# Kernel optimization log

Measured on AMD Instinct MI355X. Metric: run time of the kernel, lower is better.

Reference implementation:

```python
import jax, jax.numpy as jnp
import numpy as np

B, T, C = 2, 2048, 2048
H, D = 16, 128


def _rope(x, cos, sin):
    # x: [B,H,T,D], cos/sin: [T,D//2]
    half = x.shape[-1] // 2
    x1, x2 = x[..., :half], x[..., half:]
    c = cos[None, None, :, :]
    s = sin[None, None, :, :]
    return jnp.concatenate([x1 * c - x2 * s, x1 * s + x2 * c], axis=-1)


def setup_inputs() -> dict:
    key = jax.random.key(0)
    k1, k2, k3, k4, k5 = jax.random.split(key, 5)
    x = jax.random.normal(k1, (B, T, C), dtype=jnp.float32)
    cos = jax.random.uniform(k2, (T, D // 2), dtype=jnp.float32)
    sin = jax.random.uniform(k3, (T, D // 2), dtype=jnp.float32)
    scale = 1.0 / np.sqrt(C)
    W_qkv = jax.random.normal(k4, (C, 3 * C), dtype=jnp.float32) * scale
    W_proj = jax.random.normal(k5, (C, C), dtype=jnp.float32) * scale
    return {"x": x, "cos": cos, "sin": sin, "W_qkv": W_qkv, "W_proj": W_proj}


def reference(x, cos, sin, W_qkv, W_proj):
    Bx, Tx, Cx = x.shape
    qkv = x @ W_qkv  # [B,T,3C]
    q, k, v = jnp.split(qkv, 3, axis=-1)
    # [B,T,C] -> [B,H,T,D]
    q = q.reshape(Bx, Tx, H, D).transpose(0, 2, 1, 3)
    k = k.reshape(Bx, Tx, H, D).transpose(0, 2, 1, 3)
    v = v.reshape(Bx, Tx, H, D).transpose(0, 2, 1, 3)
    q = _rope(q, cos, sin)
    k = _rope(k, cos, sin)
    # causal SDPA
    scores = jnp.einsum("bhqd,bhkd->bhqk", q, k) / jnp.sqrt(jnp.float32(D))
    causal = jnp.tril(jnp.ones((Tx, Tx), dtype=bool))
    scores = jnp.where(causal[None, None], scores, jnp.finfo(scores.dtype).min)
    attn = jax.nn.softmax(scores, axis=-1)
    out = jnp.einsum("bhqk,bhkd->bhqd", attn, v)
    out = out.transpose(0, 2, 1, 3).reshape(Bx, Tx, Cx)
    return out @ W_proj
```

## Files before the change

### kernel.cpp

```cpp
#include <hip/hip_runtime.h>
#include <stdint.h>

#define B_  2
#define T_  2048
#define C_  2048
#define H_  16
#define D_  128
#define BH_ 32
#define M_  4096

typedef __attribute__((ext_vector_type(8))) __bf16  bf16x8;
typedef __attribute__((ext_vector_type(4))) float   floatx4;
typedef __attribute__((ext_vector_type(4))) ushort  ushortx4;

__device__ __forceinline__ ushort f2bf(float f) {
    union { float f; uint32_t u; } v; v.f = f;
    return (ushort)((v.u + 0x7fffu + ((v.u >> 16) & 1u)) >> 16);
}

__device__ __forceinline__ floatx4 mfma_bf16(bf16x8 a, bf16x8 b, floatx4 c) {
    return __builtin_amdgcn_mfma_f32_16x16x32_bf16(a, b, c, 0, 0, 0);
}

__device__ __forceinline__ void async16(const ushort* g, ushort* l) {
    __builtin_amdgcn_global_load_lds(
        (const __attribute__((address_space(1))) uint32_t*)g,
        (__attribute__((address_space(3))) uint32_t*)l, 16, 0, 0);
}

__global__ __launch_bounds__(256) void transpose_w(
    const float* __restrict__ W, ushort* __restrict__ Wt, int Kdim, int Ndim)
{
    __shared__ float tile[32][33];
    const int n0 = blockIdx.x * 32, k0 = blockIdx.y * 32;
    const int tx = threadIdx.x, ty = threadIdx.y;
    #pragma unroll
    for (int j = 0; j < 4; j++)
        tile[ty + j*8][tx] = W[(size_t)(k0 + ty + j*8) * Ndim + n0 + tx];
    __syncthreads();
    #pragma unroll
    for (int j = 0; j < 4; j++)
        Wt[(size_t)(n0 + ty + j*8) * Kdim + k0 + tx] = f2bf(tile[tx][ty + j*8]);
}

#define BM 128
#define BN 128
#define BK 32
#define LDK 40

__global__ __launch_bounds__(256) void gemm_af32_btbf16(
    const float* __restrict__ A, const ushort* __restrict__ Bt,
    float* __restrict__ Co, int Ndim, int Kdim)
{
    __shared__ __align__(16) ushort As[BM * LDK];
    __shared__ __align__(16) ushort Bs[BN * LDK];
    const int tid  = threadIdx.x;
    const int lane = tid & 63;
    const int w    = tid >> 6;
    const int wm   = (w >> 1) * 64;
    const int wn   = (w & 1) * 64;
    const int lr   = lane & 15;
    const int quad = lane >> 4;

    const float*  Ablk = A  + (size_t)(blockIdx.y * BM) * Kdim;
    const ushort* Bblk = Bt + (size_t)(blockIdx.x * BN) * Kdim;

    floatx4 acc[4][4];
    #pragma unroll
    for (int i = 0; i < 4; i++)
        #pragma unroll
        for (int j = 0; j < 4; j++)
            acc[i][j] = (floatx4){0.f, 0.f, 0.f, 0.f};

    for (int k0 = 0; k0 < Kdim; k0 += BK) {
        #pragma unroll
        for (int i = 0; i < 4; i++) {
            int idx = tid + i * 256;
            int row = idx >> 3;
            int c4  = (idx & 7) * 4;
            const float4 a = *(const float4*)(Ablk + (size_t)row * Kdim + k0 + c4);
            ushortx4 p = { f2bf(a.x), f2bf(a.y), f2bf(a.z), f2bf(a.w) };
            *(ushortx4*)(&As[row * LDK + c4]) = p;
        }
        #pragma unroll
        for (int i = 0; i < 2; i++) {
            int idx = tid + i * 256;
            int row = idx >> 2;
            int c8  = (idx & 3) * 8;
            bf16x8 bv = *(const bf16x8*)(Bblk + (size_t)row * Kdim + k0 + c8);
            *(bf16x8*)(&Bs[row * LDK + c8]) = bv;
        }
        __syncthreads();

        bf16x8 af[4], bfr[4];
        #pragma unroll
        for (int mi = 0; mi < 4; mi++)
            af[mi] = *(const bf16x8*)(&As[(wm + mi*16 + lr) * LDK + quad * 8]);
        #pragma unroll
        for (int ni = 0; ni < 4; ni++)
            bfr[ni] = *(const bf16x8*)(&Bs[(wn + ni*16 + lr) * LDK + quad * 8]);
        #pragma unroll
        for (int mi = 0; mi < 4; mi++)
            #pragma unroll
            for (int ni = 0; ni < 4; ni++)
                acc[mi][ni] = mfma_bf16(af[mi], bfr[ni], acc[mi][ni]);
        __syncthreads();
    }

    const size_t row0 = (size_t)blockIdx.y * BM + wm;
    const size_t col0 = (size_t)blockIdx.x * BN + wn;
    #pragma unroll
    for (int mi = 0; mi < 4; mi++)
        #pragma unroll
        for (int ni = 0; ni < 4; ni++)
            #pragma unroll
            for (int r = 0; r < 4; r++)
                Co[(row0 + mi*16 + quad*4 + r) * (size_t)Ndim + col0 + ni*16 + lr]
                    = acc[mi][ni][r];
}

__global__ __launch_bounds__(256) void rope_qk(
    const float* __restrict__ qkv, const float* __restrict__ cosb,
    const float* __restrict__ sinb, ushort* __restrict__ qb, ushort* __restrict__ kb)
{
    const int tid = blockIdx.x * 256 + threadIdx.x;
    const int d  = tid & 63;
    const int t  = (tid >> 6) & (T_ - 1);
    const int bh = tid >> 17;
    const int b  = bh >> 4, h = bh & 15;

    const size_t base = ((size_t)(b * T_ + t)) * (3 * C_) + h * D_;
    const float c = cosb[t * 64 + d], s = sinb[t * 64 + d];
    const float q1 = qkv[base + d],       q2 = qkv[base + d + 64];
    const float k1 = qkv[base + C_ + d],  k2 = qkv[base + C_ + d + 64];

    const size_t ob = ((size_t)bh * T_ + t) * D_;
    qb[ob + d]      = f2bf(q1 * c - q2 * s);
    qb[ob + d + 64] = f2bf(q1 * s + q2 * c);
    kb[ob + d]      = f2bf(k1 * c - k2 * s);
    kb[ob + d + 64] = f2bf(k1 * s + k2 * c);
}

__global__ __launch_bounds__(256) void transpose_v(
    const float* __restrict__ qkv, ushort* __restrict__ vt)
{
    __shared__ float tile[32][33];
    const int bh = blockIdx.y;
    const int b = bh >> 4, h = bh & 15;
    const int t0 = (blockIdx.x >> 2) * 32;
    const int d0 = (blockIdx.x & 3) * 32;
    const int tx = threadIdx.x, ty = threadIdx.y;
    #pragma unroll
    for (int j = 0; j < 4; j++) {
        int t = t0 + ty + j * 8;
        tile[ty + j*8][tx] =
            qkv[((size_t)(b * T_ + t)) * (3 * C_) + 2 * C_ + h * D_ + d0 + tx];
    }
    __syncthreads();
    #pragma unroll
    for (int j = 0; j < 4; j++) {
        int d = d0 + ty + j * 8;
        vt[((size_t)bh * D_ + d) * T_ + t0 + tx] = f2bf(tile[tx][ty + j*8]);
    }
}

__global__ __launch_bounds__(256, 4) void flash_attn(
    const ushort* __restrict__ qb, const ushort* __restrict__ kb,
    const ushort* __restrict__ vt, float* __restrict__ attnout)
{
    __shared__ __align__(16) ushort kt_s[64 * 128];
    __shared__ __align__(16) ushort vt_s[128 * 64];
    __shared__ __align__(16) ushort pl_s[4][16 * 40];

    const int w    = threadIdx.x >> 6;
    const int lane = threadIdx.x & 63;
    const int lr   = lane & 15;
    const int quad = lane >> 4;

    const int bh = blockIdx.x & 31;
    const int m  = 31 - (blockIdx.x >> 5);
    const int qt = 4 * m + w;
    const int qbase = qt * 16;
    const int nk = m + 1;
    const int bb = bh >> 4, hh = bh & 15;

    const ushort* kbp = kb + (size_t)bh * T_ * D_;
    const ushort* vbp = vt + (size_t)bh * D_ * T_;
    ushort* pl = pl_s[w];

    bf16x8 qf[4];
    const ushort* qrow = qb + ((size_t)bh * T_ + qbase + lr) * D_ + quad * 8;
    #pragma unroll
    for (int kc = 0; kc < 4; kc++)
        qf[kc] = *(const bf16x8*)(qrow + kc * 32);

    floatx4 o[8];
    #pragma unroll
    for (int dc = 0; dc < 8; dc++) o[dc] = (floatx4){0.f, 0.f, 0.f, 0.f};
    floatx4 lac = (floatx4){0.f, 0.f, 0.f, 0.f};

    const __bf16 one = (__bf16)1.0f;
    const bf16x8 ones = {one, one, one, one, one, one, one, one};
    const float SCL  = 0.08838834764831845f * 1.4426950408889634f;
    const float BIAS = 23.083120654223414f;

    const int krow4 = lane >> 4;
    const int kunit = lane & 15;
    const int vrow8 = lane >> 3;
    const int vunit = lane & 7;

    for (int kt = 0; kt < nk; ++kt) {
        const int kb0 = kt * 64;
        __syncthreads();
        #pragma unroll
        for (int j = 0; j < 4; j++) {
            const int row = w * 16 + j * 4 + krow4;
            const ushort* gp = kbp + (size_t)(kb0 + row) * D_
                                   + ((kunit ^ (row & 15)) << 3);
            async16(gp, kt_s + (w * 16 + j * 4) * 128);
        }
        #pragma unroll
        for (int j = 0; j < 4; j++) {
            const int row = w * 32 + j * 8 + vrow8;
            const ushort* gp = vbp + (size_t)row * T_ + kb0
                                   + ((vunit ^ (row & 7)) << 3);
            async16(gp, vt_s + (w * 32 + j * 8) * 64);
        }
        __syncthreads();

        #pragma unroll
        for (int half = 0; half < 2; ++half) {
            floatx4 st[2];
            #pragma unroll
            for (int jj = 0; jj < 2; ++jj) {
                const int j = half * 2 + jj;
                floatx4 s = (floatx4){0.f, 0.f, 0.f, 0.f};
                const int kl = j * 16 + lr;
                #pragma unroll
                for (int kc = 0; kc < 4; kc++) {
                    bf16x8 af = *(const bf16x8*)(
                        kt_s + kl * 128 + ((((kc << 2) | quad) ^ lr) << 3));
                    s = mfma_bf16(af, qf[kc], s);
                }
                st[jj] = s;
            }
            #pragma unroll
            for (int jj = 0; jj < 2; ++jj) {
                const int j = half * 2 + jj;
                const int kg0 = kb0 + j * 16 + quad * 4;
                float p[4];
                #pragma unroll
                for (int r = 0; r < 4; r++) {
                    float e = __builtin_amdgcn_exp2f(fmaf(st[jj][r], SCL, -BIAS));
                    p[r] = (kg0 + r > qbase + lr) ? 0.f : e;
                }
                uint2 pk;
                pk.x = (uint32_t)f2bf(p[0]) | ((uint32_t)f2bf(p[1]) << 16);
                pk.y = (uint32_t)f2bf(p[2]) | ((uint32_t)f2bf(p[3]) << 16);
                *(uint2*)(pl + lr * 40 + jj * 16 + quad * 4) = pk;
            }
            bf16x8 pf = *(const bf16x8*)(pl + lr * 40 + quad * 8);
            lac = mfma_bf16(pf, ones, lac);
            #pragma unroll
            for (int dc = 0; dc < 8; dc++) {
                const int d = dc * 16 + lr;
                bf16x8 vf = *(const bf16x8*)(
                    vt_s + d * 64 + ((((half << 2) | quad) ^ (lr & 7)) << 3));
                o[dc] = mfma_bf16(pf, vf, o[dc]);
            }
        }
    }

    #pragma unroll
    for (int dc = 0; dc < 8; dc++)
        #pragma unroll
        for (int r = 0; r < 4; r++) {
            const int trow = qbase + quad * 4 + r;
            attnout[(((size_t)(bb * T_ + trow)) * H_ + hh) * D_ + dc * 16 + lr]
                = o[dc][r] / lac[r];
        }
}

extern "C" void kernel_launch(void* const* d_in, const int* in_sizes, int n_in,
                              void* d_out, int out_size, void* d_ws, size_t ws_size,
                              hipStream_t stream)
{
    (void)in_sizes; (void)n_in; (void)out_size; (void)ws_size;
    const float* x     = (const float*)d_in[0];
    const float* cosb  = (const float*)d_in[1];
    const float* sinb  = (const float*)d_in[2];
    const float* Wqkv  = (const float*)d_in[3];
    const float* Wproj = (const float*)d_in[4];
    float* out = (float*)d_out;

    char* ws = (char*)d_ws;
    float*  qkv = (float*)(ws);
    ushort* Wtq = (ushort*)(ws + 100663296);
    ushort* Wtp = (ushort*)(ws + 125829120);
    ushort* qb  = (ushort*)(ws + 134217728);
    ushort* kbf = (ushort*)(ws + 150994944);
    ushort* vt  = (ushort*)(ws + 167772160);

    dim3 tb32(32, 8);
    transpose_w<<<dim3(3 * C_ / 32, C_ / 32), tb32, 0, stream>>>(Wqkv, Wtq, C_, 3 * C_);
    transpose_w<<<dim3(C_ / 32, C_ / 32),     tb32, 0, stream>>>(Wproj, Wtp, C_, C_);

    gemm_af32_btbf16<<<dim3(3 * C_ / BN, M_ / BM), 256, 0, stream>>>(
        x, Wtq, qkv, 3 * C_, C_);

    rope_qk<<<(BH_ * T_ * 64) / 256, 256, 0, stream>>>(qkv, cosb, sinb, qb, kbf);
    transpose_v<<<dim3((T_ / 32) * (D_ / 32), BH_), tb32, 0, stream>>>(qkv, vt);

    float* attnout = qkv;
    flash_attn<<<BH_ * 32, 256, 0, stream>>>(qb, kbf, vt, attnout);

    gemm_af32_btbf16<<<dim3(C_ / BN, M_ / BM), 256, 0, stream>>>(
        attnout, Wtp, out, C_, C_);
}
```

Before: 477.5 us.

## Pre-convert GEMM inputs to bf16 and stage tiles via direct global-to-LDS loads

Adds a separate kernel that converts x to bf16, and makes flash attention write its output directly as bf16 in [B,T,C] layout. Both GEMMs can then take bf16 A and B operands. The GEMM stages tiles with global_load_lds async copies instead of loading into registers, converting and storing to LDS. This removes the per-tile fp32-to-bf16 conversion and register round-trip and halves A-operand traffic. In exchange it drops the LDS row padding, which may add bank conflicts, and it reshuffles workspace buffers so they alias (qb over Wtq, attnoutb over qkv).

```diff
diff --git a/kernel.cpp b/kernel.cpp
--- a/kernel.cpp
+++ b/kernel.cpp
@@ -28,6 +28,15 @@
         (__attribute__((address_space(3))) uint32_t*)l, 16, 0, 0);
 }
 
+__global__ __launch_bounds__(256) void convert_bf16(
+    const float* __restrict__ X, ushort* __restrict__ Xb)
+{
+    const int i = blockIdx.x * 256 + threadIdx.x;
+    const float4 v = ((const float4*)X)[i];
+    ushortx4 p = { f2bf(v.x), f2bf(v.y), f2bf(v.z), f2bf(v.w) };
+    ((ushortx4*)Xb)[i] = p;
+}
+
 __global__ __launch_bounds__(256) void transpose_w(
     const float* __restrict__ W, ushort* __restrict__ Wt, int Kdim, int Ndim)
 {
@@ -46,14 +55,13 @@
 #define BM 128
 #define BN 128
 #define BK 32
-#define LDK 40
-
-__global__ __launch_bounds__(256) void gemm_af32_btbf16(
-    const float* __restrict__ A, const ushort* __restrict__ Bt,
+
+__global__ __launch_bounds__(256) void gemm_bt(
+    const ushort* __restrict__ A, const ushort* __restrict__ Bt,
     float* __restrict__ Co, int Ndim, int Kdim)
 {
-    __shared__ __align__(16) ushort As[BM * LDK];
-    __shared__ __align__(16) ushort Bs[BN * LDK];
+    __shared__ __align__(16) ushort As[BM * BK];
+    __shared__ __align__(16) ushort Bs[BN * BK];
     const int tid  = threadIdx.x;
     const int lane = tid & 63;
     const int w    = tid >> 6;
@@ -61,8 +69,10 @@
     const int wn   = (w & 1) * 64;
     const int lr   = lane & 15;
     const int quad = lane >> 4;
-
-    const float*  Ablk = A  + (size_t)(blockIdx.y * BM) * Kdim;
+    const int srow = lane >> 2;
+    const int soff = (lane & 3) * 8;
+
+    const ushort* Ablk = A  + (size_t)(blockIdx.y * BM) * Kdim;
     const ushort* Bblk = Bt + (size_t)(blockIdx.x * BN) * Kdim;
 
     floatx4 acc[4][4];
@@ -73,38 +83,29 @@
             acc[i][j] = (floatx4){0.f, 0.f, 0.f, 0.f};
 
     for (int k0 = 0; k0 < Kdim; k0 += BK) {
-        #pragma unroll
-        for (int i = 0; i < 4; i++) {
-            int idx = tid + i * 256;
-            int row = idx >> 3;
-            int c4  = (idx & 7) * 4;
-            const float4 a = *(const float4*)(Ablk + (size_t)row * Kdim + k0 + c4);
-            ushortx4 p = { f2bf(a.x), f2bf(a.y), f2bf(a.z), f2bf(a.w) };
-            *(ushortx4*)(&As[row * LDK + c4]) = p;
-        }
-        #pragma unroll
-        for (int i = 0; i < 2; i++) {
-            int idx = tid + i * 256;
-            int row = idx >> 2;
-            int c8  = (idx & 3) * 8;
-            bf16x8 bv = *(const bf16x8*)(Bblk + (size_t)row * Kdim + k0 + c8);
-            *(bf16x8*)(&Bs[row * LDK + c8]) = bv;
-        }
         __syncthreads();
+        #pragma unroll
+        for (int j = 0; j < 2; j++) {
+            const int row = w * 32 + j * 16 + srow;
+            async16(Ablk + (size_t)row * Kdim + k0 + soff,
+                    As + (w * 32 + j * 16) * BK);
+            async16(Bblk + (size_t)row * Kdim + k0 + soff,
+                    Bs + (w * 32 + j * 16) * BK);
+        }
+        __syncthreads();
 
         bf16x8 af[4], bfr[4];
         #pragma unroll
         for (int mi = 0; mi < 4; mi++)
-            af[mi] = *(const bf16x8*)(&As[(wm + mi*16 + lr) * LDK + quad * 8]);
+            af[mi] = *(const bf16x8*)(&As[(wm + mi*16 + lr) * BK + quad * 8]);
         #pragma unroll
         for (int ni = 0; ni < 4; ni++)
-            bfr[ni] = *(const bf16x8*)(&Bs[(wn + ni*16 + lr) * LDK + quad * 8]);
+            bfr[ni] = *(const bf16x8*)(&Bs[(wn + ni*16 + lr) * BK + quad * 8]);
         #pragma unroll
         for (int mi = 0; mi < 4; mi++)
             #pragma unroll
             for (int ni = 0; ni < 4; ni++)
                 acc[mi][ni] = mfma_bf16(af[mi], bfr[ni], acc[mi][ni]);
-        __syncthreads();
     }
 
     const size_t row0 = (size_t)blockIdx.y * BM + wm;
@@ -166,7 +167,7 @@
 
 __global__ __launch_bounds__(256, 4) void flash_attn(
     const ushort* __restrict__ qb, const ushort* __restrict__ kb,
-    const ushort* __restrict__ vt, float* __restrict__ attnout)
+    const ushort* __restrict__ vt, ushort* __restrict__ attnoutb)
 {
     __shared__ __align__(16) ushort kt_s[64 * 128];
     __shared__ __align__(16) ushort vt_s[128 * 64];
@@ -276,8 +277,8 @@
         #pragma unroll
         for (int r = 0; r < 4; r++) {
             const int trow = qbase + quad * 4 + r;
-            attnout[(((size_t)(bb * T_ + trow)) * H_ + hh) * D_ + dc * 16 + lr]
-                = o[dc][r] / lac[r];
+            attnoutb[((size_t)(bb * T_ + trow)) * C_ + hh * D_ + dc * 16 + lr]
+                = f2bf(o[dc][r] / lac[r]);
         }
 }
 
@@ -294,26 +295,26 @@
     float* out = (float*)d_out;
 
     char* ws = (char*)d_ws;
-    float*  qkv = (float*)(ws);
+    float*  qkv      = (float*)(ws);
+    ushort* attnoutb = (ushort*)(ws);
     ushort* Wtq = (ushort*)(ws + 100663296);
+    ushort* qb  = (ushort*)(ws + 100663296);
     ushort* Wtp = (ushort*)(ws + 125829120);
-    ushort* qb  = (ushort*)(ws + 134217728);
-    ushort* kbf = (ushort*)(ws + 150994944);
-    ushort* vt  = (ushort*)(ws + 167772160);
+    ushort* kbf = (ushort*)(ws + 134217728);
+    ushort* vt  = (ushort*)(ws + 150994944);
+    ushort* xb  = (ushort*)(ws + 167772160);
 
     dim3 tb32(32, 8);
     transpose_w<<<dim3(3 * C_ / 32, C_ / 32), tb32, 0, stream>>>(Wqkv, Wtq, C_, 3 * C_);
     transpose_w<<<dim3(C_ / 32, C_ / 32),     tb32, 0, stream>>>(Wproj, Wtp, C_, C_);
-
-    gemm_af32_btbf16<<<dim3(3 * C_ / BN, M_ / BM), 256, 0, stream>>>(
-        x, Wtq, qkv, 3 * C_, C_);
+    convert_bf16<<<(M_ * C_ / 4) / 256, 256, 0, stream>>>(x, xb);
+
+    gemm_bt<<<dim3(3 * C_ / BN, M_ / BM), 256, 0, stream>>>(xb, Wtq, qkv, 3 * C_, C_);
 
     rope_qk<<<(BH_ * T_ * 64) / 256, 256, 0, stream>>>(qkv, cosb, sinb, qb, kbf);
     transpose_v<<<dim3((T_ / 32) * (D_ / 32), BH_), tb32, 0, stream>>>(qkv, vt);
 
-    float* attnout = qkv;
-    flash_attn<<<BH_ * 32, 256, 0, stream>>>(qb, kbf, vt, attnout);
-
-    gemm_af32_btbf16<<<dim3(C_ / BN, M_ / BM), 256, 0, stream>>>(
-        attnout, Wtp, out, C_, C_);
-}
+    flash_attn<<<BH_ * 32, 256, 0, stream>>>(qb, kbf, vt, attnoutb);
+
+    gemm_bt<<<dim3(C_ / BN, M_ / BM), 256, 0, stream>>>(attnoutb, Wtp, out, C_, C_);
+}
```

Result: faster. 427.0 us (-10.6%).
